# Optimization experiments

Hardware: AMD Instinct MI355X
Metric: run time of the kernel (lower is better)

The kernel has to match this reference:

```python
import jax, jax.numpy as jnp
import numpy as np

B, S, D, HID, H, VOCAB, DFF = 4, 2048, 512, 512, 8, 32000, 2048
DK = HID // H   # per-head Q/K dim
DV = D // H     # per-head V dim


def sinusoidal_pe(L, d):
    pos = jnp.arange(L, dtype=jnp.float32)[:, None]
    i = jnp.arange(d, dtype=jnp.float32)[None, :]
    ang = pos / jnp.power(jnp.float32(10000.0), i / d)
    return jnp.where(jnp.arange(d)[None, :] % 2 == 0, jnp.sin(ang), jnp.cos(ang))  # [L, d]


def layer_norm(x, gamma, beta, eps=1e-5):
    mu = jnp.mean(x, axis=-1, keepdims=True)
    var = jnp.mean((x - mu) ** 2, axis=-1, keepdims=True)
    return (x - mu) * jax.lax.rsqrt(var + eps) * gamma + beta


def setup_inputs() -> dict:
    key = jax.random.key(0)
    ks = jax.random.split(key, 24)
    n = lambda k, shape, fan: jax.random.normal(k, shape, dtype=jnp.float32) / np.sqrt(fan)
    inp = {
        'x': jax.random.randint(ks[0], (B, S), 0, VOCAB),
        'emb': n(ks[1], (VOCAB, D), D),
        'WfQ': n(ks[2], (D, HID), D), 'bfQ': jnp.zeros((HID,), jnp.float32),
        'WfK': n(ks[3], (D, HID), D), 'bfK': jnp.zeros((HID,), jnp.float32),
        'WfV': n(ks[4], (D, D), D),   'bfV': jnp.zeros((D,), jnp.float32),
        'WQ': n(ks[5], (H, HID, DK), HID), 'bQ': jnp.zeros((H, DK), jnp.float32),
        'WK': n(ks[6], (H, HID, DK), HID), 'bK': jnp.zeros((H, DK), jnp.float32),
        'WV': n(ks[7], (H, D, DV), D),     'bV': jnp.zeros((H, DV), jnp.float32),
        'Wo': n(ks[8], (D, D), D),   'bo': jnp.zeros((D,), jnp.float32),
        'W1': n(ks[9], (D, DFF), D), 'b1': jnp.zeros((DFF,), jnp.float32),
        'W2': n(ks[10], (DFF, D), DFF), 'b2': jnp.zeros((D,), jnp.float32),
        'gamma': jnp.ones((D,), jnp.float32), 'beta': jnp.zeros((D,), jnp.float32),
    }
    return inp


def reference(x, emb, WfQ, bfQ, WfK, bfK, WfV, bfV, WQ, bQ, WK, bK, WV, bV,
              Wo, bo, W1, b1, W2, b2, gamma, beta):
    z = emb[x] + sinusoidal_pe(x.shape[1], D)[None]            # [B,S,D]
    Q = z @ WfQ + bfQ                                           # [B,S,HID]
    K = z @ WfK + bfK
    V = z @ WfV + bfV                                           # [B,S,D]
    # per-head projections (batched equivalent of the per-head Linear loop)
    Qh = jnp.einsum('bsd,hdk->bhsk', Q, WQ) + bQ[None, :, None, :]  # [B,H,S,DK]
    Kh = jnp.einsum('bsd,hdk->bhsk', K, WK) + bK[None, :, None, :]
    Vh = jnp.einsum('bsd,hdv->bhsv', V, WV) + bV[None, :, None, :]  # [B,H,S,DV]
    scores = jnp.einsum('bhqk,bhsk->bhqs', Qh, Kh) / np.sqrt(DK)    # [B,H,S,S]
    attn = jax.nn.softmax(scores, axis=-1)
    heads = jnp.einsum('bhqs,bhsv->bhqv', attn, Vh)                 # [B,H,S,DV]
    concat = heads.transpose(0, 2, 1, 3).reshape(x.shape[0], x.shape[1], D)
    attn_out = concat @ Wo + bo
    a = layer_norm(attn_out + z, gamma, beta)
    ffn = jax.nn.relu(a @ W1 + b1) @ W2 + b2
    out = layer_norm(ffn + a, gamma, beta)   # same (shared) LayerNorm params, as in source
    return jax.nn.relu(out)
```

## Files before the change

### kernel.cpp

```cpp
#include <hip/hip_runtime.h>
#include <math.h>

typedef __bf16 bf16;
typedef __bf16 bf16x8 __attribute__((ext_vector_type(8)));
typedef __bf16 bf16x4 __attribute__((ext_vector_type(4)));
typedef _Float16 f16;
typedef _Float16 f16x8 __attribute__((ext_vector_type(8)));
typedef _Float16 f16x4 __attribute__((ext_vector_type(4)));
typedef _Float16 f16x2 __attribute__((ext_vector_type(2)));
typedef __fp16 h16x2 __attribute__((ext_vector_type(2)));
typedef float f32x4 __attribute__((ext_vector_type(4)));
typedef unsigned int u32;

#define S_LEN 2048
#define QSCALE 0.18033688011112042f

#if __has_builtin(__builtin_amdgcn_exp2f)
#define EXP2(x) __builtin_amdgcn_exp2f(x)
#else
#define EXP2(x) exp2f(x)
#endif

__device__ __forceinline__ void gload_lds16(const void* g, void* l) {
  __builtin_amdgcn_global_load_lds((const __attribute__((address_space(1))) u32*)g,
                                   (__attribute__((address_space(3))) u32*)l, 16, 0, 0);
}

__global__ __launch_bounds__(256) void embed_pe(const int* __restrict__ x,
    const float* __restrict__ emb, bf16* __restrict__ zb)
{
  const int row = blockIdx.x;
  const int s = row & (S_LEN - 1);
  const int tok = x[row];
  const float* e = emb + (size_t)tok * 512;
  bf16* zbr = zb + (size_t)row * 512;
  for (int i = threadIdx.x; i < 512; i += 256) {
    float invf = __expf((float)i * (-9.210340371976184f / 512.0f));
    float ang = (float)s * invf;
    float pe = (i & 1) ? __cosf(ang) : __sinf(ang);
    zbr[i] = (bf16)(e[i] + pe);
  }
}

__global__ __launch_bounds__(256) void conv_all(
    const float* __restrict__ WfQ, const float* __restrict__ WfK, const float* __restrict__ WfV,
    const float* __restrict__ WQ, const float* __restrict__ WK, const float* __restrict__ WV,
    const float* __restrict__ Wo, const float* __restrict__ W1, const float* __restrict__ W2,
    bf16* __restrict__ wfqp, bf16* __restrict__ wfkp, bf16* __restrict__ wfvp,
    bf16* __restrict__ wqt, bf16* __restrict__ wkt, bf16* __restrict__ wvt,
    bf16* __restrict__ wot, bf16* __restrict__ w1t, bf16* __restrict__ w2t)
{
  int gid = blockIdx.x * 256 + threadIdx.x;
  int y = blockIdx.y;
  if (y < 3) {
    if (gid >= 262144) return;
    const float* in = y == 0 ? WfQ : (y == 1 ? WfK : WfV);
    bf16* out = y == 0 ? wfqp : (y == 1 ? wfkp : wfvp);
    out[gid] = (bf16)in[gid];
  } else if (y < 6) {
    if (gid >= 262144) return;
    const float* in = y == 3 ? WQ : (y == 4 ? WK : WV);
    bf16* out = y == 3 ? wqt : (y == 4 ? wkt : wvt);
    float scale = y == 3 ? QSCALE : 1.0f;
    int r = gid & 511, t = gid >> 9, c = t & 63, h = t >> 6;
    out[gid] = (bf16)(in[((size_t)(h * 512 + r)) * 64 + c] * scale);
  } else if (y == 6) {
    if (gid >= 262144) return;
    int r = gid & 511, c = gid >> 9;
    wot[gid] = (bf16)Wo[r * 512 + c];
  } else if (y == 7) {
    int r = gid & 511, c = gid >> 9;
    w1t[gid] = (bf16)W1[r * 2048 + c];
  } else {
    int r = gid & 2047, c = gid >> 11;
    w2t[gid] = (bf16)W2[r * 512 + c];
  }
}

__global__ __launch_bounds__(256) void bias_comb(
    const float* __restrict__ bfQ, const float* __restrict__ bfK, const float* __restrict__ bfV,
    const float* __restrict__ WQ, const float* __restrict__ WK, const float* __restrict__ WV,
    const float* __restrict__ bQ, const float* __restrict__ bK, const float* __restrict__ bV,
    float* __restrict__ bc)
{
  int n = blockIdx.x * 4 + (threadIdx.x >> 6);
  int lane = threadIdx.x & 63;
  int z = n >> 9, hk = n & 511, h = hk >> 6, k = hk & 63;
  const float* bf = z == 0 ? bfQ : (z == 1 ? bfK : bfV);
  const float* W  = z == 0 ? WQ  : (z == 1 ? WK  : WV);
  const float* bH = z == 0 ? bQ  : (z == 1 ? bK  : bV);
  float s = 0.f;
  for (int e = lane; e < 512; e += 64)
    s += bf[e] * W[((size_t)h * 512 + e) * 64 + k];
  #pragma unroll
  for (int m = 1; m < 64; m <<= 1) s += __shfl_xor(s, m, 64);
  if (lane == 0) {
    float v = s + bH[h * 64 + k];
    if (z == 0) v *= QSCALE;
    bc[n] = v;
  }
}

__global__ __launch_bounds__(256) void gemm_comb(
    const bf16* __restrict__ wqt, const bf16* __restrict__ wkt, const bf16* __restrict__ wvt,
    const bf16* __restrict__ wfqp, const bf16* __restrict__ wfkp, const bf16* __restrict__ wfvp,
    bf16* __restrict__ wc)
{
  __shared__ bf16 As[128 * 32];
  __shared__ bf16 Bs[64 * 32];
  const int z = blockIdx.z;
  const bf16* A  = z == 0 ? wqt : (z == 1 ? wkt : wvt);
  const bf16* Bt = z == 0 ? wfqp : (z == 1 ? wfkp : wfvp);
  bf16* outb = wc + (size_t)z * 262144;
  const int tid = threadIdx.x;
  const int wave = tid >> 6, lane = tid & 63, quad = lane >> 4, l16 = lane & 15;
  const int row0 = blockIdx.x * 128, col0 = blockIdx.y * 64;
  const int wm = wave >> 1, wn = wave & 1;
  f32x4 acc[4][2] = {};

  for (int kk = 0; kk < 512; kk += 32) {
    __syncthreads();
    #pragma unroll
    for (int r = 0; r < 2; r++) {
      int c = r * 256 + tid;
      gload_lds16(A + (size_t)(row0 + (c >> 2)) * 512 + kk + (c & 3) * 8, As + c * 8);
    }
    gload_lds16(Bt + (size_t)(col0 + (tid >> 2)) * 512 + kk + (tid & 3) * 8, Bs + tid * 8);
    __syncthreads();
    bf16x8 af[4], bfr[2];
    #pragma unroll
    for (int i = 0; i < 4; i++)
      af[i] = *(const bf16x8*)(As + (wm * 64 + i * 16 + l16) * 32 + quad * 8);
    #pragma unroll
    for (int i = 0; i < 2; i++)
      bfr[i] = *(const bf16x8*)(Bs + (wn * 32 + i * 16 + l16) * 32 + quad * 8);
    #pragma unroll
    for (int mt = 0; mt < 4; mt++)
      #pragma unroll
      for (int nt = 0; nt < 2; nt++)
        acc[mt][nt] = __builtin_amdgcn_mfma_f32_16x16x32_bf16(af[mt], bfr[nt], acc[mt][nt], 0, 0, 0);
  }
  #pragma unroll
  for (int nt = 0; nt < 2; nt++) {
    int col = col0 + wn * 32 + nt * 16 + l16;
    #pragma unroll
    for (int mt = 0; mt < 4; mt++) {
      int rowb = row0 + wm * 64 + mt * 16 + quad * 4;
      #pragma unroll
      for (int i = 0; i < 4; i++)
        outb[(size_t)(rowb + i) * 512 + col] = (bf16)acc[mt][nt][i];
    }
  }
}

#define GEMM_CORE(A_, Bt_, K_, KK0_, ITERS_)                                            \
  bf16x8 ar0, ar1, br0, br1;                                                            \
  const int c0 = tid, c1 = 256 + tid;                                                   \
  const size_t aoff0 = (size_t)(row0 + (c0 >> 2)) * (K_) + (c0 & 3) * 8;                \
  const size_t aoff1 = (size_t)(row0 + (c1 >> 2)) * (K_) + (c1 & 3) * 8;                \
  const size_t boff0 = (size_t)(col0 + (c0 >> 2)) * (K_) + (c0 & 3) * 8;                \
  const size_t boff1 = (size_t)(col0 + (c1 >> 2)) * (K_) + (c1 & 3) * 8;                \
  ar0 = *(const bf16x8*)((A_) + aoff0 + (KK0_));                                        \
  ar1 = *(const bf16x8*)((A_) + aoff1 + (KK0_));                                        \
  br0 = *(const bf16x8*)((Bt_) + boff0 + (KK0_));                                       \
  br1 = *(const bf16x8*)((Bt_) + boff1 + (KK0_));                                       \
  for (int it = 0; it < (ITERS_); it++) {                                               \
    bf16* AsB = As[it & 1];                                                             \
    bf16* BsB = Bs[it & 1];                                                             \
    *(bf16x8*)(AsB + c0 * 8) = ar0;                                                     \
    *(bf16x8*)(AsB + c1 * 8) = ar1;                                                     \
    *(bf16x8*)(BsB + c0 * 8) = br0;                                                     \
    *(bf16x8*)(BsB + c1 * 8) = br1;                                                     \
    __syncthreads();                                                                    \
    if (it + 1 < (ITERS_)) {                                                            \
      int kk = (KK0_) + (it + 1) * 32;                                                  \
      ar0 = *(const bf16x8*)((A_) + aoff0 + kk);                                        \
      ar1 = *(const bf16x8*)((A_) + aoff1 + kk);                                        \
      br0 = *(const bf16x8*)((Bt_) + boff0 + kk);                                       \
      br1 = *(const bf16x8*)((Bt_) + boff1 + kk);                                       \
    }                                                                                   \
    bf16x8 af[4], bfr[4];                                                               \
    _Pragma("unroll")                                                                   \
    for (int i = 0; i < 4; i++)                                                         \
      af[i] = *(const bf16x8*)(AsB + (wm * 64 + i * 16 + l16) * 32 + quad * 8);         \
    _Pragma("unroll")                                                                   \
    for (int i = 0; i < 4; i++)                                                         \
      bfr[i] = *(const bf16x8*)(BsB + (wn * 64 + i * 16 + l16) * 32 + quad * 8);        \
    _Pragma("unroll")                                                                   \
    for (int mt = 0; mt < 4; mt++)                                                      \
      _Pragma("unroll")                                                                 \
      for (int nt = 0; nt < 4; nt++)                                                    \
        acc[mt][nt] = __builtin_amdgcn_mfma_f32_16x16x32_bf16(af[mt], bfr[nt], acc[mt][nt], 0, 0, 0); \
  }

__global__ __launch_bounds__(256) void gemm_bt(
    const bf16* __restrict__ A, const bf16* __restrict__ Bt,
    const float* __restrict__ bias, bf16* __restrict__ outb,
    int M, int N, int K, int relu)
{
  __shared__ bf16 As[2][4096];
  __shared__ bf16 Bs[2][4096];
  const int tid = threadIdx.x;
  const int wave = tid >> 6, lane = tid & 63, quad = lane >> 4, l16 = lane & 15;
  const int row0 = blockIdx.x * 128, col0 = blockIdx.y * 128;
  const int wm = wave >> 1, wn = wave & 1;
  f32x4 acc[4][4] = {};
  GEMM_CORE(A, Bt, K, 0, K / 32)

  #pragma unroll
  for (int nt = 0; nt < 4; nt++) {
    int col = col0 + wn * 64 + nt * 16 + l16;
    float bv = bias[col];
    #pragma unroll
    for (int mt = 0; mt < 4; mt++) {
      int rowb = row0 + wm * 64 + mt * 16 + quad * 4;
      #pragma unroll
      for (int i = 0; i < 4; i++) {
        float v = acc[mt][nt][i] + bv;
        if (relu) v = fmaxf(v, 0.f);
        outb[(size_t)(rowb + i) * N + col] = (bf16)v;
      }
    }
  }
}

__global__ __launch_bounds__(256) void gemm_qkv(
    const bf16* __restrict__ A, const bf16* __restrict__ Bt,
    const float* __restrict__ bias, f16* __restrict__ qk, f16* __restrict__ Vt)
{
  __shared__ bf16 As[2][4096];
  __shared__ bf16 Bs[2][4096];
  const int tid = threadIdx.x;
  const int wave = tid >> 6, lane = tid & 63, quad = lane >> 4, l16 = lane & 15;
  const int row0 = blockIdx.x * 128, col0 = blockIdx.y * 128;
  const int wm = wave >> 1, wn = wave & 1;
  f32x4 acc[4][4] = {};
  GEMM_CORE(A, Bt, 512, 0, 16)

  #pragma unroll
  for (int nt = 0; nt < 4; nt++) {
    int col = col0 + wn * 64 + nt * 16 + l16;
    float bv = bias[col];
    if (col < 1024) {
      #pragma unroll
      for (int mt = 0; mt < 4; mt++) {
        int rowb = row0 + wm * 64 + mt * 16 + quad * 4;
        #pragma unroll
        for (int i = 0; i < 4; i++)
          qk[(size_t)(rowb + i) * 1024 + col] = (f16)(acc[mt][nt][i] + bv);
      }
    } else {
      int h = (col - 1024) >> 6, dv = col & 63;
      #pragma unroll
      for (int mt = 0; mt < 4; mt++) {
        int rowb = row0 + wm * 64 + mt * 16 + quad * 4;
        int b = rowb >> 11, s = rowb & 2047;
        f16x4 vv;
        #pragma unroll
        for (int i = 0; i < 4; i++) vv[i] = (f16)(acc[mt][nt][i] + bv);
        *(f16x4*)(Vt + ((size_t)((b * 8 + h) * 64 + dv)) * 2048 + s) = vv;
      }
    }
  }
}

__global__ __launch_bounds__(256) void gemm_part(
    const bf16* __restrict__ A, const bf16* __restrict__ Bt,
    bf16* __restrict__ Pa, bf16* __restrict__ Pb, int N, int K, int Kh)
{
  __shared__ bf16 As[2][4096];
  __shared__ bf16 Bs[2][4096];
  const int tid = threadIdx.x;
  const int wave = tid >> 6, lane = tid & 63, quad = lane >> 4, l16 = lane & 15;
  const int row0 = blockIdx.x * 128, col0 = blockIdx.y * 128;
  const int wm = wave >> 1, wn = wave & 1;
  const int kk0 = blockIdx.z * Kh;
  bf16* P = blockIdx.z ? Pb : Pa;
  f32x4 acc[4][4] = {};
  GEMM_CORE(A, Bt, K, kk0, Kh / 32)

  #pragma unroll
  for (int nt = 0; nt < 4; nt++) {
    int col = col0 + wn * 64 + nt * 16 + l16;
    #pragma unroll
    for (int mt = 0; mt < 4; mt++) {
      int rowb = row0 + wm * 64 + mt * 16 + quad * 4;
      #pragma unroll
      for (int i = 0; i < 4; i++)
        P[(size_t)(rowb + i) * N + col] = (bf16)acc[mt][nt][i];
    }
  }
}

__global__ __launch_bounds__(256) void flash_attn(
    const f16* __restrict__ qk, const f16* __restrict__ Vt,
    bf16* __restrict__ Op, float* __restrict__ Rp)
{
  __shared__ f16 Ks[2][4096];
  __shared__ f16 Vs[2][4096];
  const int bh = blockIdx.y, b = bh >> 3, h = bh & 7;
  const int q0 = blockIdx.x * 128;
  const int quarter = blockIdx.z;
  const int tid = threadIdx.x;
  const int wave = tid >> 6, lane = tid & 63, quad = lane >> 4, l16 = lane & 15;

  const f16* Qb = qk + ((size_t)b * S_LEN) * 1024 + h * 64;
  const f16* Kb = Qb + 512;
  const f16* Vtb = Vt + ((size_t)bh * 64) * 2048;
  const int key0 = quarter * 512;

  f16x8 qf[2][2];
  #pragma unroll
  for (int f = 0; f < 2; f++) {
    int qrow = q0 + wave * 32 + f * 16 + l16;
    #pragma unroll
    for (int kh = 0; kh < 2; kh++)
      qf[f][kh] = *(const f16x8*)(Qb + (size_t)qrow * 1024 + kh * 32 + quad * 8);
  }

  f32x4 O[2][4] = {};
  f32x4 Osum[2] = {};
  const f16x4 onesA = {(f16)1.f, (f16)1.f, (f16)1.f, (f16)1.f};
  const int swz = l16 & 7;

  f16x8 kreg[2], vreg[2];
  const int srow = tid >> 3, soff = tid & 7;
  const int srow1 = srow + 32;

  {
    int kb = key0;
    kreg[0] = *(const f16x8*)(Kb + (size_t)(kb + srow) * 1024 + soff * 8);
    vreg[0] = *(const f16x8*)(Vtb + (size_t)srow * 2048 + kb + soff * 8);
    kreg[1] = *(const f16x8*)(Kb + (size_t)(kb + srow1) * 1024 + soff * 8);
    vreg[1] = *(const f16x8*)(Vtb + (size_t)srow1 * 2048 + kb + soff * 8);
  }

  for (int c = 0; c < 8; c++) {
    f16* KsB = Ks[c & 1];
    f16* VsB = Vs[c & 1];
    *(f16x8*)(KsB + srow * 64 + ((soff ^ (srow & 7)) * 8)) = kreg[0];
    *(f16x8*)(VsB + srow * 64 + ((soff ^ (srow & 7)) * 8)) = vreg[0];
    *(f16x8*)(KsB + srow1 * 64 + ((soff ^ (srow1 & 7)) * 8)) = kreg[1];
    *(f16x8*)(VsB + srow1 * 64 + ((soff ^ (srow1 & 7)) * 8)) = vreg[1];
    __syncthreads();
    if (c < 7) {
      int kb = key0 + (c + 1) * 64;
      kreg[0] = *(const f16x8*)(Kb + (size_t)(kb + srow) * 1024 + soff * 8);
      vreg[0] = *(const f16x8*)(Vtb + (size_t)srow * 2048 + kb + soff * 8);
      kreg[1] = *(const f16x8*)(Kb + (size_t)(kb + srow1) * 1024 + soff * 8);
      vreg[1] = *(const f16x8*)(Vtb + (size_t)srow1 * 2048 + kb + soff * 8);
    }

    #pragma unroll
    for (int nt = 0; nt < 4; nt++) {
      const f16* kp = KsB + (nt * 16 + l16) * 64;
      f16x8 kf0 = *(const f16x8*)(kp + ((quad ^ swz) * 8));
      f16x8 kf1 = *(const f16x8*)(kp + (((4 + quad) ^ swz) * 8));
      f16x4 pf[2];
      #pragma unroll
      for (int f = 0; f < 2; f++) {
        f32x4 a = {};
        a = __builtin_amdgcn_mfma_f32_16x16x32_f16(kf0, qf[f][0], a, 0, 0, 0);
        a = __builtin_amdgcn_mfma_f32_16x16x32_f16(kf1, qf[f][1], a, 0, 0, 0);
        float e0 = EXP2(a[0]);
        float e1 = EXP2(a[1]);
        float e2 = EXP2(a[2]);
        float e3 = EXP2(a[3]);
        h16x2 lo = __builtin_amdgcn_cvt_pkrtz(e0, e1);
        h16x2 hi = __builtin_amdgcn_cvt_pkrtz(e2, e3);
        f16x2 lo2 = __builtin_bit_cast(f16x2, lo);
        f16x2 hi2 = __builtin_bit_cast(f16x2, hi);
        pf[f] = __builtin_shufflevector(lo2, hi2, 0, 1, 2, 3);
        Osum[f] = __builtin_amdgcn_mfma_f32_16x16x16f16(onesA, pf[f], Osum[f], 0, 0, 0);
      }
      int vchunk = nt * 2 + (quad >> 1);
      #pragma unroll
      for (int mt = 0; mt < 4; mt++) {
        const f16* vp = VsB + (mt * 16 + l16) * 64 + ((vchunk ^ swz) * 8) + (quad & 1) * 4;
        f16x4 vf = *(const f16x4*)vp;
        #pragma unroll
        for (int f = 0; f < 2; f++)
          O[f][mt] = __builtin_amdgcn_mfma_f32_16x16x16f16(vf, pf[f], O[f][mt], 0, 0, 0);
      }
    }
  }

  #pragma unroll
  for (int f = 0; f < 2; f++) {
    bf16* ob = (f == 0 ? (bf16*)&Ks[0][0] : (bf16*)&Vs[0][0]) + wave * 1024;
    #pragma unroll
    for (int mt = 0; mt < 4; mt++) {
      bf16x4 w;
      #pragma unroll
      for (int i = 0; i < 4; i++) w[i] = (bf16)O[f][mt][i];
      int chunk = mt * 2 + (quad >> 1);
      *(bf16x4*)(ob + l16 * 64 + ((chunk ^ (l16 & 7)) << 3) + (quad & 1) * 4) = w;
    }
  }
  asm volatile("s_waitcnt lgkmcnt(0)" ::: "memory");
  const size_t obase = (size_t)(quarter * 32 + bh) * 2048;
  #pragma unroll
  for (int f = 0; f < 2; f++) {
    const bf16* ob = (f == 0 ? (const bf16*)&Ks[0][0] : (const bf16*)&Vs[0][0]) + wave * 1024;
    int row = lane >> 2, c0 = (lane & 3) * 2;
    bf16x8 o0 = *(const bf16x8*)(ob + row * 64 + ((c0 ^ (row & 7)) << 3));
    bf16x8 o1 = *(const bf16x8*)(ob + row * 64 + (((c0 + 1) ^ (row & 7)) << 3));
    size_t g = (obase + q0 + wave * 32 + f * 16 + row) * 64 + (lane & 3) * 16;
    *(bf16x8*)(Op + g) = o0;
    *(bf16x8*)(Op + g + 8) = o1;
    if (quad == f)
      Rp[obase + q0 + wave * 32 + f * 16 + l16] = Osum[f][0];
  }
}

__global__ __launch_bounds__(256) void attn_merge(const bf16* __restrict__ Op,
    const float* __restrict__ Rp, bf16* __restrict__ concat)
{
  int t = blockIdx.x * 256 + threadIdx.x;
  int dv4 = t & 15, s = (t >> 4) & 2047, bh = t >> 15;
  int rb = bh * 2048 + s;
  float r = (Rp[rb] + Rp[65536 + rb]) + (Rp[131072 + rb] + Rp[196608 + rb]);
  float inv = 1.f / r;
  size_t ia = ((size_t)bh * 2048 + s) * 64 + dv4 * 4;
  bf16x4 p0 = *(const bf16x4*)(Op + ia);
  bf16x4 p1 = *(const bf16x4*)(Op + 4194304ull + ia);
  bf16x4 p2 = *(const bf16x4*)(Op + 8388608ull + ia);
  bf16x4 p3 = *(const bf16x4*)(Op + 12582912ull + ia);
  bf16x4 o;
  #pragma unroll
  for (int i = 0; i < 4; i++)
    o[i] = (bf16)((((float)p0[i] + (float)p1[i]) + ((float)p2[i] + (float)p3[i])) * inv);
  int b = bh >> 3, h = bh & 7;
  *(bf16x4*)(concat + ((size_t)(b * 2048 + s)) * 512 + h * 64 + dv4 * 4) = o;
}

__global__ __launch_bounds__(256) void ln_merge(const bf16* __restrict__ Pa,
    const bf16* __restrict__ Pb, const float* __restrict__ badd,
    const bf16* __restrict__ resid, const float* __restrict__ gamma,
    const float* __restrict__ beta, float* __restrict__ outf,
    bf16* __restrict__ outb, int relu)
{
  const int row = blockIdx.x * 4 + (threadIdx.x >> 6);
  const int lane = threadIdx.x & 63;
  const size_t base = (size_t)row * 512;
  const int e0 = lane * 8;
  bf16x8 pa = *(const bf16x8*)(Pa + base + e0);
  bf16x8 pb = *(const bf16x8*)(Pb + base + e0);
  bf16x8 rr = *(const bf16x8*)(resid + base + e0);
  float4 C0 = *(const float4*)(badd + e0);
  float4 C1 = *(const float4*)(badd + e0 + 4);
  float v[8];
  v[0] = (float)pa[0] + (float)pb[0] + (float)rr[0] + C0.x;
  v[1] = (float)pa[1] + (float)pb[1] + (float)rr[1] + C0.y;
  v[2] = (float)pa[2] + (float)pb[2] + (float)rr[2] + C0.z;
  v[3] = (float)pa[3] + (float)pb[3] + (float)rr[3] + C0.w;
  v[4] = (float)pa[4] + (float)pb[4] + (float)rr[4] + C1.x;
  v[5] = (float)pa[5] + (float)pb[5] + (float)rr[5] + C1.y;
  v[6] = (float)pa[6] + (float)pb[6] + (float)rr[6] + C1.z;
  v[7] = (float)pa[7] + (float)pb[7] + (float)rr[7] + C1.w;
  float s = 0.f;
  #pragma unroll
  for (int i = 0; i < 8; i++) s += v[i];
  #pragma unroll
  for (int m = 1; m < 64; m <<= 1) s += __shfl_xor(s, m, 64);
  float mu = s * (1.f / 512.f);
  float d[8], q = 0.f;
  #pragma unroll
  for (int i = 0; i < 8; i++) { d[i] = v[i] - mu; q += d[i] * d[i]; }
  #pragma unroll
  for (int m = 1; m < 64; m <<= 1) q += __shfl_xor(q, m, 64);
  float rs = rsqrtf(q * (1.f / 512.f) + 1e-5f);
  float4 g0 = *(const float4*)(gamma + e0);
  float4 g1 = *(const float4*)(gamma + e0 + 4);
  float4 b0 = *(const float4*)(beta + e0);
  float4 b1 = *(const float4*)(beta + e0 + 4);
  float y[8];
  y[0] = d[0] * rs * g0.x + b0.x; y[1] = d[1] * rs * g0.y + b0.y;
  y[2] = d[2] * rs * g0.z + b0.z; y[3] = d[3] * rs * g0.w + b0.w;
  y[4] = d[4] * rs * g1.x + b1.x; y[5] = d[5] * rs * g1.y + b1.y;
  y[6] = d[6] * rs * g1.z + b1.z; y[7] = d[7] * rs * g1.w + b1.w;
  if (relu) {
    #pragma unroll
    for (int i = 0; i < 8; i++) y[i] = fmaxf(y[i], 0.f);
  }
  if (outf) {
    float4 o0 = {y[0], y[1], y[2], y[3]}, o1 = {y[4], y[5], y[6], y[7]};
    *(float4*)(outf + base + e0) = o0;
    *(float4*)(outf + base + e0 + 4) = o1;
  }
  if (outb) {
    bf16x8 ob;
    #pragma unroll
    for (int i = 0; i < 8; i++) ob[i] = (bf16)y[i];
    *(bf16x8*)(outb + base + e0) = ob;
  }
}

extern "C" void kernel_launch(void* const* d_in, const int* in_sizes, int n_in,
                              void* d_out, int out_size, void* d_ws, size_t ws_size,
                              hipStream_t stream)
{
  const int*   x    = (const int*)  d_in[0];
  const float* emb  = (const float*)d_in[1];
  const float* WfQ  = (const float*)d_in[2];
  const float* bfQv = (const float*)d_in[3];
  const float* WfK  = (const float*)d_in[4];
  const float* bfKv = (const float*)d_in[5];
  const float* WfV  = (const float*)d_in[6];
  const float* bfVv = (const float*)d_in[7];
  const float* WQ   = (const float*)d_in[8];
  const float* bQ   = (const float*)d_in[9];
  const float* WK   = (const float*)d_in[10];
  const float* bK   = (const float*)d_in[11];
  const float* WV   = (const float*)d_in[12];
  const float* bV   = (const float*)d_in[13];
  const float* Wo   = (const float*)d_in[14];
  const float* bo   = (const float*)d_in[15];
  const float* W1   = (const float*)d_in[16];
  const float* b1   = (const float*)d_in[17];
  const float* W2   = (const float*)d_in[18];
  const float* b2   = (const float*)d_in[19];
  const float* gamma= (const float*)d_in[20];
  const float* beta = (const float*)d_in[21];
  float* out = (float*)d_out;

  char* ws = (char*)d_ws;
  const size_t MB = 1024ull * 1024;
  bf16*  bz   = (bf16*) (ws);
  f16*   qkh  = (f16*)  (ws + 8 * MB);
  f16*   Vt   = (f16*)  (ws + 24 * MB);
  bf16*  Op   = (bf16*) (ws + 32 * MB);
  float* Rp   = (float*)(ws + 64 * MB);
  bf16*  concat = (bf16*)(ws + 66 * MB);
  bf16*  PaW  = (bf16*) (ws + 32 * MB);
  bf16*  PbW  = (bf16*) (ws + 40 * MB);
  bf16*  ffn1 = (bf16*) (ws + 8 * MB);
  bf16*  Pa2  = (bf16*) (ws + 40 * MB);
  bf16*  Pb2  = (bf16*) (ws + 48 * MB);
  char* wp = ws + 74 * MB;
  bf16* wfqp = (bf16*)(wp);
  bf16* wfkp = (bf16*)(wp + 512 * 1024);
  bf16* wfvp = (bf16*)(wp + 1024 * 1024);
  bf16* wqt  = (bf16*)(wp + 1536 * 1024);
  bf16* wkt  = (bf16*)(wp + 2048 * 1024);
  bf16* wvt  = (bf16*)(wp + 2560 * 1024);
  bf16* wc   = (bf16*)(wp + 3072 * 1024);
  bf16* wot  = (bf16*)(wp + 4608 * 1024);
  bf16* w1t  = (bf16*)(wp + 5120 * 1024);
  bf16* w2t  = (bf16*)(wp + 7168 * 1024);
  float* bc  = (float*)(wp + 9216 * 1024);

  conv_all<<<dim3(4096, 9), 256, 0, stream>>>(WfQ, WfK, WfV, WQ, WK, WV, Wo, W1, W2,
                                              wfqp, wfkp, wfvp, wqt, wkt, wvt, wot, w1t, w2t);
  bias_comb<<<384, 256, 0, stream>>>(bfQv, bfKv, bfVv, WQ, WK, WV, bQ, bK, bV, bc);
  gemm_comb<<<dim3(4, 8, 3), 256, 0, stream>>>(wqt, wkt, wvt, wfqp, wfkp, wfvp, wc);

  embed_pe<<<8192, 256, 0, stream>>>(x, emb, bz);

  gemm_qkv<<<dim3(64, 12), 256, 0, stream>>>(bz, wc, bc, qkh, Vt);
  flash_attn<<<dim3(16, 32, 4), 256, 0, stream>>>(qkh, Vt, Op, Rp);
  attn_merge<<<4096, 256, 0, stream>>>(Op, Rp, concat);

  gemm_part<<<dim3(64, 4, 2), 256, 0, stream>>>(concat, wot, PaW, PbW, 512, 512, 256);
  ln_merge<<<2048, 256, 0, stream>>>(PaW, PbW, bo, bz, gamma, beta, nullptr, bz, 0);
  gemm_bt<<<dim3(64, 16), 256, 0, stream>>>(bz, w1t, b1, ffn1, 8192, 2048, 512, 1);
  gemm_part<<<dim3(64, 4, 2), 256, 0, stream>>>(ffn1, w2t, Pa2, Pb2, 512, 2048, 1024);
  ln_merge<<<2048, 256, 0, stream>>>(Pa2, Pb2, b2, bz, gamma, beta, out, nullptr, 1);
}
```

Before: 338.9 us.

## Tile weight transposes in LDS, halve attention key splits, use dot2 rowsums

Replaces the monolithic weight conversion kernel with a vectorized copy kernel and an LDS-tiled transpose kernel, so fp32 weight reads are coalesced. Changes flash attention from four key splits of 512 to two splits of 1024. This halves partial output traffic and the merge work but leaves fewer blocks for parallelism. Replaces the MFMA-with-ones row-sum with fdot2 accumulation plus cross-lane shuffles, freeing matrix-core cycles.

```diff
diff --git a/kernel.cpp b/kernel.cpp
--- a/kernel.cpp
+++ b/kernel.cpp
@@ -42,38 +42,61 @@
   }
 }
 
-__global__ __launch_bounds__(256) void conv_all(
+__global__ __launch_bounds__(256) void conv_copy(
     const float* __restrict__ WfQ, const float* __restrict__ WfK, const float* __restrict__ WfV,
+    bf16* __restrict__ wfqp, bf16* __restrict__ wfkp, bf16* __restrict__ wfvp)
+{
+  int g = blockIdx.x * 256 + threadIdx.x;
+  const float* in = blockIdx.y == 0 ? WfQ : (blockIdx.y == 1 ? WfK : WfV);
+  bf16* out = blockIdx.y == 0 ? wfqp : (blockIdx.y == 1 ? wfkp : wfvp);
+  float4 v = *(const float4*)(in + (size_t)g * 4);
+  bf16x4 o = {(bf16)v.x, (bf16)v.y, (bf16)v.z, (bf16)v.w};
+  *(bf16x4*)(out + (size_t)g * 4) = o;
+}
+
+__global__ __launch_bounds__(256) void conv_t(
+    const float* __restrict__ Wo, const float* __restrict__ W1, const float* __restrict__ W2,
     const float* __restrict__ WQ, const float* __restrict__ WK, const float* __restrict__ WV,
-    const float* __restrict__ Wo, const float* __restrict__ W1, const float* __restrict__ W2,
-    bf16* __restrict__ wfqp, bf16* __restrict__ wfkp, bf16* __restrict__ wfvp,
-    bf16* __restrict__ wqt, bf16* __restrict__ wkt, bf16* __restrict__ wvt,
-    bf16* __restrict__ wot, bf16* __restrict__ w1t, bf16* __restrict__ w2t)
-{
-  int gid = blockIdx.x * 256 + threadIdx.x;
-  int y = blockIdx.y;
-  if (y < 3) {
-    if (gid >= 262144) return;
-    const float* in = y == 0 ? WfQ : (y == 1 ? WfK : WfV);
-    bf16* out = y == 0 ? wfqp : (y == 1 ? wfkp : wfvp);
-    out[gid] = (bf16)in[gid];
-  } else if (y < 6) {
-    if (gid >= 262144) return;
-    const float* in = y == 3 ? WQ : (y == 4 ? WK : WV);
-    bf16* out = y == 3 ? wqt : (y == 4 ? wkt : wvt);
-    float scale = y == 3 ? QSCALE : 1.0f;
-    int r = gid & 511, t = gid >> 9, c = t & 63, h = t >> 6;
-    out[gid] = (bf16)(in[((size_t)(h * 512 + r)) * 64 + c] * scale);
-  } else if (y == 6) {
-    if (gid >= 262144) return;
-    int r = gid & 511, c = gid >> 9;
-    wot[gid] = (bf16)Wo[r * 512 + c];
-  } else if (y == 7) {
-    int r = gid & 511, c = gid >> 9;
-    w1t[gid] = (bf16)W1[r * 2048 + c];
+    bf16* __restrict__ wot, bf16* __restrict__ w1t, bf16* __restrict__ w2t,
+    bf16* __restrict__ wqt, bf16* __restrict__ wkt, bf16* __restrict__ wvt)
+{
+  __shared__ float T[64][65];
+  const int y = blockIdx.y, x = blockIdx.x;
+  const int tx = threadIdx.x & 63, ty = threadIdx.x >> 6;
+  const float* src; bf16* dst;
+  int src_cols, dst_cols; float scale = 1.f;
+  if (y == 0) {
+    if (x >= 64) return;
+    int kt = x & 7, nt = x >> 3;
+    src = Wo + (size_t)(kt * 64) * 512 + nt * 64; src_cols = 512;
+    dst = wot + (size_t)(nt * 64) * 512 + kt * 64; dst_cols = 512;
+  } else if (y == 1) {
+    int kt = x & 7, nt = x >> 3;
+    src = W1 + (size_t)(kt * 64) * 2048 + nt * 64; src_cols = 2048;
+    dst = w1t + (size_t)(nt * 64) * 512 + kt * 64; dst_cols = 512;
+  } else if (y == 2) {
+    int kt = x & 31, nt = x >> 5;
+    src = W2 + (size_t)(kt * 64) * 512 + nt * 64; src_cols = 512;
+    dst = w2t + (size_t)(nt * 64) * 2048 + kt * 64; dst_cols = 2048;
   } else {
-    int r = gid & 2047, c = gid >> 11;
-    w2t[gid] = (bf16)W2[r * 512 + c];
+    if (x >= 64) return;
+    const float* W = y == 3 ? WQ : (y == 4 ? WK : WV);
+    bf16* o = y == 3 ? wqt : (y == 4 ? wkt : wvt);
+    if (y == 3) scale = QSCALE;
+    int h = x >> 3, rt = x & 7;
+    src = W + (size_t)(h * 512 + rt * 64) * 64; src_cols = 64;
+    dst = o + (size_t)(h * 64) * 512 + rt * 64; dst_cols = 512;
+  }
+  #pragma unroll
+  for (int i = 0; i < 16; i++) {
+    int rr = i * 4 + ty;
+    T[rr][tx] = src[(size_t)rr * src_cols + tx];
+  }
+  __syncthreads();
+  #pragma unroll
+  for (int i = 0; i < 16; i++) {
+    int rr = i * 4 + ty;
+    dst[(size_t)rr * dst_cols + tx] = (bf16)(T[tx][rr] * scale);
   }
 }
 
@@ -176,8 +199,8 @@
       int kk = (KK0_) + (it + 1) * 32;                                                  \
       ar0 = *(const bf16x8*)((A_) + aoff0 + kk);                                        \
       ar1 = *(const bf16x8*)((A_) + aoff1 + kk);                                        \
-      br0 = *(const bf16x8*)((Bt_) + boff0 + kk);                                       \
-      br1 = *(const bf16x8*)((Bt_) + boff1 + kk);                                       \
+      br0 = *(const bf16x8*)((Bt_) + boff0 + kk);                                      \
+      br1 = *(const bf16x8*)((Bt_) + boff1 + kk);                                      \
     }                                                                                   \
     bf16x8 af[4], bfr[4];                                                               \
     _Pragma("unroll")                                                                   \
@@ -307,7 +330,7 @@
   const f16* Qb = qk + ((size_t)b * S_LEN) * 1024 + h * 64;
   const f16* Kb = Qb + 512;
   const f16* Vtb = Vt + ((size_t)bh * 64) * 2048;
-  const int key0 = quarter * 512;
+  const int key0 = quarter * 1024;
 
   f16x8 qf[2][2];
   #pragma unroll
@@ -319,8 +342,7 @@
   }
 
   f32x4 O[2][4] = {};
-  f32x4 Osum[2] = {};
-  const f16x4 onesA = {(f16)1.f, (f16)1.f, (f16)1.f, (f16)1.f};
+  float rs[2] = {0.f, 0.f};
   const int swz = l16 & 7;
 
   f16x8 kreg[2], vreg[2];
@@ -335,7 +357,7 @@
     vreg[1] = *(const f16x8*)(Vtb + (size_t)srow1 * 2048 + kb + soff * 8);
   }
 
-  for (int c = 0; c < 8; c++) {
+  for (int c = 0; c < 16; c++) {
     f16* KsB = Ks[c & 1];
     f16* VsB = Vs[c & 1];
     *(f16x8*)(KsB + srow * 64 + ((soff ^ (srow & 7)) * 8)) = kreg[0];
@@ -343,7 +365,7 @@
     *(f16x8*)(KsB + srow1 * 64 + ((soff ^ (srow1 & 7)) * 8)) = kreg[1];
     *(f16x8*)(VsB + srow1 * 64 + ((soff ^ (srow1 & 7)) * 8)) = vreg[1];
     __syncthreads();
-    if (c < 7) {
+    if (c < 15) {
       int kb = key0 + (c + 1) * 64;
       kreg[0] = *(const f16x8*)(Kb + (size_t)(kb + srow) * 1024 + soff * 8);
       vreg[0] = *(const f16x8*)(Vtb + (size_t)srow * 2048 + kb + soff * 8);
@@ -371,7 +393,13 @@
         f16x2 lo2 = __builtin_bit_cast(f16x2, lo);
         f16x2 hi2 = __builtin_bit_cast(f16x2, hi);
         pf[f] = __builtin_shufflevector(lo2, hi2, 0, 1, 2, 3);
-        Osum[f] = __builtin_amdgcn_mfma_f32_16x16x16f16(onesA, pf[f], Osum[f], 0, 0, 0);
+#if __has_builtin(__builtin_amdgcn_fdot2)
+        const f16x2 ones2 = {(f16)1.f, (f16)1.f};
+        rs[f] = __builtin_amdgcn_fdot2(lo2, ones2, rs[f], false);
+        rs[f] = __builtin_amdgcn_fdot2(hi2, ones2, rs[f], false);
+#else
+        rs[f] += (e0 + e1) + (e2 + e3);
+#endif
       }
       int vchunk = nt * 2 + (quad >> 1);
       #pragma unroll
@@ -387,6 +415,12 @@
 
   #pragma unroll
   for (int f = 0; f < 2; f++) {
+    rs[f] += __shfl_xor(rs[f], 16, 64);
+    rs[f] += __shfl_xor(rs[f], 32, 64);
+  }
+
+  #pragma unroll
+  for (int f = 0; f < 2; f++) {
     bf16* ob = (f == 0 ? (bf16*)&Ks[0][0] : (bf16*)&Vs[0][0]) + wave * 1024;
     #pragma unroll
     for (int mt = 0; mt < 4; mt++) {
@@ -402,14 +436,14 @@
   #pragma unroll
   for (int f = 0; f < 2; f++) {
     const bf16* ob = (f == 0 ? (const bf16*)&Ks[0][0] : (const bf16*)&Vs[0][0]) + wave * 1024;
-    int row = lane >> 2, c0 = (lane & 3) * 2;
-    bf16x8 o0 = *(const bf16x8*)(ob + row * 64 + ((c0 ^ (row & 7)) << 3));
-    bf16x8 o1 = *(const bf16x8*)(ob + row * 64 + (((c0 + 1) ^ (row & 7)) << 3));
+    int row = lane >> 2, cc = (lane & 3) * 2;
+    bf16x8 o0 = *(const bf16x8*)(ob + row * 64 + ((cc ^ (row & 7)) << 3));
+    bf16x8 o1 = *(const bf16x8*)(ob + row * 64 + (((cc + 1) ^ (row & 7)) << 3));
     size_t g = (obase + q0 + wave * 32 + f * 16 + row) * 64 + (lane & 3) * 16;
     *(bf16x8*)(Op + g) = o0;
     *(bf16x8*)(Op + g + 8) = o1;
     if (quad == f)
-      Rp[obase + q0 + wave * 32 + f * 16 + l16] = Osum[f][0];
+      Rp[obase + q0 + wave * 32 + f * 16 + l16] = rs[f];
   }
 }
 
@@ -419,17 +453,15 @@
   int t = blockIdx.x * 256 + threadIdx.x;
   int dv4 = t & 15, s = (t >> 4) & 2047, bh = t >> 15;
   int rb = bh * 2048 + s;
-  float r = (Rp[rb] + Rp[65536 + rb]) + (Rp[131072 + rb] + Rp[196608 + rb]);
+  float r = Rp[rb] + Rp[65536 + rb];
   float inv = 1.f / r;
   size_t ia = ((size_t)bh * 2048 + s) * 64 + dv4 * 4;
   bf16x4 p0 = *(const bf16x4*)(Op + ia);
   bf16x4 p1 = *(const bf16x4*)(Op + 4194304ull + ia);
-  bf16x4 p2 = *(const bf16x4*)(Op + 8388608ull + ia);
-  bf16x4 p3 = *(const bf16x4*)(Op + 12582912ull + ia);
   bf16x4 o;
   #pragma unroll
   for (int i = 0; i < 4; i++)
-    o[i] = (bf16)((((float)p0[i] + (float)p1[i]) + ((float)p2[i] + (float)p3[i])) * inv);
+    o[i] = (bf16)(((float)p0[i] + (float)p1[i]) * inv);
   int b = bh >> 3, h = bh & 7;
   *(bf16x4*)(concat + ((size_t)(b * 2048 + s)) * 512 + h * 64 + dv4 * 4) = o;
 }
@@ -469,16 +501,16 @@
   for (int i = 0; i < 8; i++) { d[i] = v[i] - mu; q += d[i] * d[i]; }
   #pragma unroll
   for (int m = 1; m < 64; m <<= 1) q += __shfl_xor(q, m, 64);
-  float rs = rsqrtf(q * (1.f / 512.f) + 1e-5f);
+  float rsn = rsqrtf(q * (1.f / 512.f) + 1e-5f);
   float4 g0 = *(const float4*)(gamma + e0);
   float4 g1 = *(const float4*)(gamma + e0 + 4);
   float4 b0 = *(const float4*)(beta + e0);
   float4 b1 = *(const float4*)(beta + e0 + 4);
   float y[8];
-  y[0] = d[0] * rs * g0.x + b0.x; y[1] = d[1] * rs * g0.y + b0.y;
-  y[2] = d[2] * rs * g0.z + b0.z; y[3] = d[3] * rs * g0.w + b0.w;
-  y[4] = d[4] * rs * g1.x + b1.x; y[5] = d[5] * rs * g1.y + b1.y;
-  y[6] = d[6] * rs * g1.z + b1.z; y[7] = d[7] * rs * g1.w + b1.w;
+  y[0] = d[0] * rsn * g0.x + b0.x; y[1] = d[1] * rsn * g0.y + b0.y;
+  y[2] = d[2] * rsn * g0.z + b0.z; y[3] = d[3] * rsn * g0.w + b0.w;
+  y[4] = d[4] * rsn * g1.x + b1.x; y[5] = d[5] * rsn * g1.y + b1.y;
+  y[6] = d[6] * rsn * g1.z + b1.z; y[7] = d[7] * rsn * g1.w + b1.w;
   if (relu) {
     #pragma unroll
     for (int i = 0; i < 8; i++) y[i] = fmaxf(y[i], 0.f);
@@ -550,15 +582,16 @@
   bf16* w2t  = (bf16*)(wp + 7168 * 1024);
   float* bc  = (float*)(wp + 9216 * 1024);
 
-  conv_all<<<dim3(4096, 9), 256, 0, stream>>>(WfQ, WfK, WfV, WQ, WK, WV, Wo, W1, W2,
-                                              wfqp, wfkp, wfvp, wqt, wkt, wvt, wot, w1t, w2t);
+  conv_copy<<<dim3(256, 3), 256, 0, stream>>>(WfQ, WfK, WfV, wfqp, wfkp, wfvp);
+  conv_t<<<dim3(256, 6), 256, 0, stream>>>(Wo, W1, W2, WQ, WK, WV,
+                                           wot, w1t, w2t, wqt, wkt, wvt);
   bias_comb<<<384, 256, 0, stream>>>(bfQv, bfKv, bfVv, WQ, WK, WV, bQ, bK, bV, bc);
   gemm_comb<<<dim3(4, 8, 3), 256, 0, stream>>>(wqt, wkt, wvt, wfqp, wfkp, wfvp, wc);
 
   embed_pe<<<8192, 256, 0, stream>>>(x, emb, bz);
 
   gemm_qkv<<<dim3(64, 12), 256, 0, stream>>>(bz, wc, bc, qkh, Vt);
-  flash_attn<<<dim3(16, 32, 4), 256, 0, stream>>>(qkh, Vt, Op, Rp);
+  flash_attn<<<dim3(16, 32, 2), 256, 0, stream>>>(qkh, Vt, Op, Rp);
   attn_merge<<<4096, 256, 0, stream>>>(Op, Rp, concat);
 
   gemm_part<<<dim3(64, 4, 2), 256, 0, stream>>>(concat, wot, PaW, PbW, 512, 512, 256);
```

Measured after the change: 328.7 us. 3.0% less time.
